# Optimization experiments

Hardware: AMD Instinct MI355X
Metric: run time of the kernel (lower is better)

## Reference

```python
import jax, jax.numpy as jnp
import numpy as np
from jax import lax

DIM = 192
HEADS = 8
WIN = 16
B, H, W = 4, 256, 256


def setup_inputs() -> dict:
    key = jax.random.key(0)
    ks = jax.random.split(key, 8)
    s = 0.02
    return {
        "x": jax.random.normal(ks[0], (B, H, W, DIM), dtype=jnp.float32),
        "ln_g": jnp.ones((DIM,), jnp.float32),
        "ln_b": jnp.zeros((DIM,), jnp.float32),
        "wq1": jax.random.normal(ks[1], (DIM, DIM), jnp.float32) * s,
        "wq2": jax.random.normal(ks[2], (DIM, 1, 3, 3), jnp.float32) * s,
        "wk1": jax.random.normal(ks[3], (DIM, DIM), jnp.float32) * s,
        "wk2": jax.random.normal(ks[4], (DIM, 1, 3, 3), jnp.float32) * s,
        "wv1": jax.random.normal(ks[5], (DIM, DIM), jnp.float32) * s,
        "wv2": jax.random.normal(ks[6], (DIM, 1, 3, 3), jnp.float32) * s,
        "rescale": jnp.ones((HEADS, 1, 1), jnp.float32),
        "w_out": jax.random.normal(ks[7], (DIM, DIM), jnp.float32) * s,
    }


def _layernorm(x, g, b, eps=1e-5):
    mu = jnp.mean(x, axis=-1, keepdims=True)
    var = jnp.var(x, axis=-1, keepdims=True)
    return (x - mu) * lax.rsqrt(var + eps) * g + b


def _qkv(x_nchw, w1, w2):
    # 1x1 pointwise conv (no bias) as GEMM, then 3x3 depthwise conv (groups=dim)
    y = jnp.einsum('oi,bihw->bohw', w1, x_nchw)
    return lax.conv_general_dilated(
        y, w2, window_strides=(1, 1), padding='SAME',
        feature_group_count=DIM,
        dimension_numbers=('NCHW', 'OIHW', 'NCHW'))


def _windows(t):
    # [b,c,H,W] -> [b, nW, heads, d, n]   (nW = num_h*num_w, n = Wh*Ww)
    b = t.shape[0]
    nh, nw = H // WIN, W // WIN
    t = t.reshape(b, DIM, nh, WIN, nw, WIN)
    t = t.transpose(0, 1, 2, 4, 3, 5).reshape(b, DIM, nh * nw, WIN * WIN)
    d = DIM // HEADS
    t = t.reshape(b, HEADS, d, nh * nw, WIN * WIN)
    return t.transpose(0, 3, 1, 2, 4)  # b N h d n


def reference(x, ln_g, ln_b, wq1, wq2, wk1, wk2, wv1, wv2, rescale, w_out):
    b, h, w, c = x.shape
    xn = _layernorm(x, ln_g, ln_b)
    xc = xn.transpose(0, 3, 1, 2)  # NCHW
    q = _windows(_qkv(xc, wq1, wq2))
    k = _windows(_qkv(xc, wk1, wk2))
    v = _windows(_qkv(xc, wv1, wv2))
    # spectral (channel-wise) attention inside each window
    sim = jnp.einsum('bNhin,bNhjn->bNhij', q, k) * rescale
    attn = jax.nn.softmax(sim, axis=-1)
    out = jnp.einsum('bNhij,bNhjn->bNhin', attn, v)  # [b,N,h,d,n]
    # merge heads, un-window
    nh, nw = h // WIN, w // WIN
    out = out.transpose(0, 2, 3, 1, 4).reshape(b, c, nh * nw, WIN * WIN)
    out = out.reshape(b, c, nh, nw, WIN, WIN).transpose(0, 1, 2, 4, 3, 5).reshape(b, c, h, w)
    out = jnp.einsum('oi,bihw->bohw', w_out, out)
    return out.transpose(0, 2, 3, 1)  # [b,h,w,c]
```

## Files before the change

kernel.cpp:

```cpp
#include <hip/hip_runtime.h>
#include <hip/hip_bf16.h>

#define CH    192
#define NB    4
#define NHH   256
#define NWW   256
#define NPOS  (NB*NHH*NWW)
#define HEADS 8
#define DH    24
#define WIN   16
#define PS    ((size_t)NPOS*DH)

typedef unsigned short u16;
typedef __bf16 bf16x8 __attribute__((ext_vector_type(8)));
typedef float  f32x4  __attribute__((ext_vector_type(4)));
typedef u16    u16x8  __attribute__((ext_vector_type(8)));
typedef u16    u16x4  __attribute__((ext_vector_type(4)));

__device__ __forceinline__ float b2f(u16 h) {
    union { unsigned int u; float f; } x; x.u = ((unsigned int)h) << 16; return x.f;
}
__device__ __forceinline__ u16 f2b(float f) {
    union { float f; unsigned int u; } x; x.f = f;
    return (u16)((x.u + 0x7fffu + ((x.u >> 16) & 1u)) >> 16);
}

__global__ __launch_bounds__(256) void prep_weights(
    const float* __restrict__ w0, const float* __restrict__ w1,
    const float* __restrict__ w2, const float* __restrict__ w3,
    u16* __restrict__ pack)
{
    const int t = blockIdx.x * 256 + threadIdx.x;
    const int lane = t & 63, g = t >> 6;
    const int mat = g / 72;
    const float* w = (mat == 0) ? w0 : (mat == 1) ? w1 : (mat == 2) ? w2 : w3;
    const int nt = (g / 6) % 12, ks = g % 6;
    const float* src = w + (nt*16 + (lane & 15)) * CH + ks*32 + (lane >> 4) * 8;
    const float4 a = *(const float4*)(src);
    const float4 b = *(const float4*)(src + 4);
    u16x8 o;
    o[0]=f2b(a.x); o[1]=f2b(a.y); o[2]=f2b(a.z); o[3]=f2b(a.w);
    o[4]=f2b(b.x); o[5]=f2b(b.y); o[6]=f2b(b.z); o[7]=f2b(b.w);
    *(u16x8*)(pack + (size_t)g*512 + lane*8) = o;
}

__global__ __launch_bounds__(256, 6) void ln_qkv_gemm(
    const float* __restrict__ x, const float* __restrict__ lng, const float* __restrict__ lnb,
    const u16* __restrict__ bpack,
    u16* __restrict__ y0, u16* __restrict__ y1, u16* __restrict__ y2)
{
    __shared__ __align__(16) u16 At[32*192];
    __shared__ __align__(16) u16 St32[32*200];
    const int t = threadIdx.x, l = t & 63, w = t >> 6;
    const int lr = l & 15, lg = l >> 4;
    const size_t p0 = (size_t)blockIdx.x * 32;

    {
        const int row = t >> 3, part = t & 7;
        const float* xp = x + (p0 + row) * CH + part * 24;
        float vals[24];
#pragma unroll
        for (int j = 0; j < 6; ++j) {
            float4 v4 = *(const float4*)(xp + j * 4);
            vals[j*4+0]=v4.x; vals[j*4+1]=v4.y; vals[j*4+2]=v4.z; vals[j*4+3]=v4.w;
        }
        float s = 0.f, s2 = 0.f;
#pragma unroll
        for (int j = 0; j < 24; ++j) { s += vals[j]; s2 += vals[j]*vals[j]; }
        s += __shfl_xor(s, 1);  s2 += __shfl_xor(s2, 1);
        s += __shfl_xor(s, 2);  s2 += __shfl_xor(s2, 2);
        s += __shfl_xor(s, 4);  s2 += __shfl_xor(s2, 4);
        const float mu = s * (1.f/192.f);
        const float rs = rsqrtf(s2 * (1.f/192.f) - mu*mu + 1e-5f);
#pragma unroll
        for (int jb = 0; jb < 3; ++jb) {
            u16x8 o;
#pragma unroll
            for (int j = 0; j < 8; ++j) {
                const int c = part*24 + jb*8 + j;
                o[j] = f2b((vals[jb*8+j] - mu) * rs * lng[c] + lnb[c]);
            }
            const int cb = part*3 + jb;
            *(u16x8*)&At[row*192 + (cb ^ (row & 7))*8] = o;
        }
    }
    __syncthreads();

    for (int mat = 0; mat < 3; ++mat) {
        u16* yb = (mat == 0) ? y0 : (mat == 1) ? y1 : y2;
        f32x4 acc[2][3];
#pragma unroll
        for (int mt = 0; mt < 2; ++mt)
#pragma unroll
            for (int nt = 0; nt < 3; ++nt) acc[mt][nt] = (f32x4){0.f,0.f,0.f,0.f};
        const u16* bp = bpack + (size_t)mat*36864 + (size_t)w*3*3072 + l*8;
#pragma unroll
        for (int ks = 0; ks < 6; ++ks) {
            bf16x8 wf[3], xf[2];
#pragma unroll
            for (int nt = 0; nt < 3; ++nt)
                wf[nt] = *(const bf16x8*)(bp + (size_t)nt*3072 + ks*512);
#pragma unroll
            for (int mt = 0; mt < 2; ++mt)
                xf[mt] = *(const bf16x8*)&At[(mt*16 + lr)*192 + ((ks*4 + lg) ^ (lr & 7))*8];
#pragma unroll
            for (int mt = 0; mt < 2; ++mt)
#pragma unroll
                for (int nt = 0; nt < 3; ++nt)
                    acc[mt][nt] = __builtin_amdgcn_mfma_f32_16x16x32_bf16(
                        wf[nt], xf[mt], acc[mt][nt], 0, 0, 0);
        }
        __syncthreads();
#pragma unroll
        for (int mt = 0; mt < 2; ++mt)
#pragma unroll
            for (int nt = 0; nt < 3; ++nt) {
                u16x4 pk;
                pk[0] = f2b(acc[mt][nt][0]); pk[1] = f2b(acc[mt][nt][1]);
                pk[2] = f2b(acc[mt][nt][2]); pk[3] = f2b(acc[mt][nt][3]);
                *(u16x4*)&St32[(mt*16 + lr)*200 + (w*3 + nt)*16 + lg*4] = pk;
            }
        __syncthreads();
        {
            const int hh = t >> 5, r = t & 31;
            u16* dst = yb + (size_t)hh*PS + (p0 + r)*DH;
#pragma unroll
            for (int j8 = 0; j8 < 3; ++j8)
                *(u16x8*)(dst + j8*8) = *(const u16x8*)&St32[r*200 + hh*24 + j8*8];
        }
    }
}

__global__ __launch_bounds__(256) void dwconv_all(
    const u16* __restrict__ in0, const u16* __restrict__ in1, const u16* __restrict__ in2,
    const float* __restrict__ w0, const float* __restrict__ w1, const float* __restrict__ w2,
    u16* __restrict__ out0, u16* __restrict__ out1, u16* __restrict__ out2)
{
    __shared__ float wloc[DH*9];
    const int z = blockIdx.z;
    const u16* in  = (z == 0) ? in0  : (z == 1) ? in1  : in2;
    const float* wdw = (z == 0) ? w0 : (z == 1) ? w1 : w2;
    u16* out       = (z == 0) ? out0 : (z == 1) ? out1 : out2;
    const int t = threadIdx.x;
    const int h = blockIdx.y;
    if (t < DH*9) wloc[t] = wdw[h*DH*9 + t];
    __syncthreads();
    const int NSLICE = NPOS*3/256;
    const int CPX = NSLICE/8;
    const int bx = blockIdx.x;
    const int swz = (bx & 7)*CPX + (bx >> 3);
    const int gid2 = swz * 256 + t;
    const int p  = gid2 / 3, c8 = gid2 - p*3;
    const int x = p & 255, y = (p >> 8) & 255, b = p >> 16;
    const size_t plane = (size_t)h * PS;
    float acc[8] = {0,0,0,0,0,0,0,0};
#pragma unroll
    for (int ky = 0; ky < 3; ++ky) {
        const int yy = y + ky - 1;
        if (yy < 0 || yy >= NHH) continue;
#pragma unroll
        for (int kx = 0; kx < 3; ++kx) {
            const int xx = x + kx - 1;
            if (xx < 0 || xx >= NWW) continue;
            const u16x8 iv = *(const u16x8*)(in + plane + (size_t)((b*NHH + yy)*NWW + xx)*DH + c8*8);
#pragma unroll
            for (int j = 0; j < 8; ++j)
                acc[j] += b2f(iv[j]) * wloc[(c8*8 + j)*9 + ky*3 + kx];
        }
    }
    u16x8 ov;
#pragma unroll
    for (int j = 0; j < 8; ++j) ov[j] = f2b(acc[j]);
    *(u16x8*)(out + plane + (size_t)p*DH + c8*8) = ov;
}

__global__ __launch_bounds__(256) void attn_kernel(
    const u16* __restrict__ q, const u16* __restrict__ k, const u16* __restrict__ v,
    const float* __restrict__ rescale, u16* __restrict__ out)
{
    __shared__ float qt[DH][260];
    __shared__ float kt[DH][260];
    float* pbuf = &kt[0][0];
    const int t    = threadIdx.x;
    const int widx = blockIdx.x;
    const int h    = blockIdx.y;
    const int b  = widx >> 8;
    const int wy = (widx >> 4) & 15, wx = widx & 15;
    const int n  = t;
    const int gy = wy*WIN + (n >> 4), gx = wx*WIN + (n & 15);
    const size_t pbase = (size_t)h*PS + (size_t)((b*NHH + gy)*NWW + gx) * DH;

#pragma unroll
    for (int j8 = 0; j8 < 3; ++j8) {
        const u16x8 qv = *(const u16x8*)(q + pbase + j8*8);
        const u16x8 kv = *(const u16x8*)(k + pbase + j8*8);
#pragma unroll
        for (int j = 0; j < 8; ++j) { qt[j8*8+j][n] = b2f(qv[j]); kt[j8*8+j][n] = b2f(kv[j]); }
    }
    __syncthreads();

    const int wvi  = t >> 6;
    const int lane = t & 63;
    const int i0 = (lane >> 3) * 3, j0 = (lane & 7) * 3;
    float s[3][3];
#pragma unroll
    for (int a2 = 0; a2 < 3; ++a2)
#pragma unroll
        for (int c = 0; c < 3; ++c) s[a2][c] = 0.f;
    for (int nn = wvi*64; nn < wvi*64 + 64; nn += 4) {
        float4 qv[3], kv[3];
#pragma unroll
        for (int a2 = 0; a2 < 3; ++a2) {
            qv[a2] = *(const float4*)&qt[i0+a2][nn];
            kv[a2] = *(const float4*)&kt[j0+a2][nn];
        }
#pragma unroll
        for (int a2 = 0; a2 < 3; ++a2)
#pragma unroll
            for (int c = 0; c < 3; ++c)
                s[a2][c] += qv[a2].x*kv[c].x + qv[a2].y*kv[c].y + qv[a2].z*kv[c].z + qv[a2].w*kv[c].w;
    }
    __syncthreads();

#pragma unroll
    for (int a2 = 0; a2 < 3; ++a2)
#pragma unroll
        for (int c = 0; c < 3; ++c)
            pbuf[wvi*576 + (i0+a2)*24 + (j0+c)] = s[a2][c];
#pragma unroll
    for (int j8 = 0; j8 < 3; ++j8) {
        const u16x8 vv = *(const u16x8*)(v + pbase + j8*8);
#pragma unroll
        for (int j = 0; j < 8; ++j) qt[j8*8+j][n] = b2f(vv[j]);
    }
    __syncthreads();

    const float rsc = rescale[h];
    for (int e = t; e < 576; e += 256) {
        const float sum = pbuf[e] + pbuf[576+e] + pbuf[1152+e] + pbuf[1728+e];
        pbuf[2304 + e] = sum * rsc;
    }
    __syncthreads();

    if (t < 24) {
        float* srow = pbuf + 2304 + t*24;
        float m = srow[0];
#pragma unroll
        for (int j = 1; j < 24; ++j) m = fmaxf(m, srow[j]);
        float ssum = 0.f;
#pragma unroll
        for (int j = 0; j < 24; ++j) { const float e_ = expf(srow[j] - m); srow[j] = e_; ssum += e_; }
        const float inv = 1.f / ssum;
#pragma unroll
        for (int j = 0; j < 24; ++j) srow[j] *= inv;
    }
    __syncthreads();

    const int nc = t & 63;
    const int ib = (t >> 6) * 6;
    float4 acc[6];
#pragma unroll
    for (int ii = 0; ii < 6; ++ii) acc[ii] = make_float4(0.f,0.f,0.f,0.f);
#pragma unroll
    for (int j = 0; j < 24; ++j) {
        const float4 vj = *(const float4*)&qt[j][nc*4];
        const float aw0 = pbuf[2304 + (ib+0)*24 + j];
        const float aw1 = pbuf[2304 + (ib+1)*24 + j];
        const float aw2 = pbuf[2304 + (ib+2)*24 + j];
        const float aw3 = pbuf[2304 + (ib+3)*24 + j];
        const float aw4 = pbuf[2304 + (ib+4)*24 + j];
        const float aw5 = pbuf[2304 + (ib+5)*24 + j];
        acc[0].x += aw0*vj.x; acc[0].y += aw0*vj.y; acc[0].z += aw0*vj.z; acc[0].w += aw0*vj.w;
        acc[1].x += aw1*vj.x; acc[1].y += aw1*vj.y; acc[1].z += aw1*vj.z; acc[1].w += aw1*vj.w;
        acc[2].x += aw2*vj.x; acc[2].y += aw2*vj.y; acc[2].z += aw2*vj.z; acc[2].w += aw2*vj.w;
        acc[3].x += aw3*vj.x; acc[3].y += aw3*vj.y; acc[3].z += aw3*vj.z; acc[3].w += aw3*vj.w;
        acc[4].x += aw4*vj.x; acc[4].y += aw4*vj.y; acc[4].z += aw4*vj.z; acc[4].w += aw4*vj.w;
        acc[5].x += aw5*vj.x; acc[5].y += aw5*vj.y; acc[5].z += aw5*vj.z; acc[5].w += aw5*vj.w;
    }
    __syncthreads();
#pragma unroll
    for (int ii = 0; ii < 6; ++ii)
        *(float4*)&qt[ib+ii][nc*4] = acc[ii];
    __syncthreads();
#pragma unroll
    for (int j8 = 0; j8 < 3; ++j8) {
        u16x8 o;
#pragma unroll
        for (int j = 0; j < 8; ++j) o[j] = f2b(qt[j8*8+j][n]);
        *(u16x8*)(out + pbase + j8*8) = o;
    }
}

__global__ __launch_bounds__(256) void outproj_gemm(
    const u16* __restrict__ a, const u16* __restrict__ bpack, float* __restrict__ yf)
{
    __shared__ __align__(16) u16 At[64*192];
    __shared__ __align__(16) float Sf[32*196];
    const int t = threadIdx.x, l = t & 63, w = t >> 6;
    const int lr = l & 15, lg = l >> 4;
    const size_t p0 = (size_t)blockIdx.x * 64;

#pragma unroll
    for (int i = 0; i < 6; ++i) {
        const int idx = t + i*256;
        const int h = idx / 192;
        const int rem = idx - h*192;
        const int r = rem / 3, c8 = rem - r*3;
        const u16x8 vv = *(const u16x8*)(a + (size_t)h*PS + (p0 + r)*DH + c8*8);
        *(u16x8*)&At[r*192 + (((h*3 + c8) ^ (r & 7))*8)] = vv;
    }
    __syncthreads();

    f32x4 acc[4][3];
#pragma unroll
    for (int mt = 0; mt < 4; ++mt)
#pragma unroll
        for (int nt = 0; nt < 3; ++nt) acc[mt][nt] = (f32x4){0.f,0.f,0.f,0.f};
    const u16* bp = bpack + (size_t)3*36864 + (size_t)w*3*3072 + l*8;
#pragma unroll
    for (int ks = 0; ks < 6; ++ks) {
        bf16x8 af[4], bfr[3];
#pragma unroll
        for (int nt = 0; nt < 3; ++nt)
            bfr[nt] = *(const bf16x8*)(bp + (size_t)nt*3072 + ks*512);
#pragma unroll
        for (int mt = 0; mt < 4; ++mt)
            af[mt] = *(const bf16x8*)&At[(mt*16 + lr)*192 + ((ks*4 + lg) ^ (lr & 7))*8];
#pragma unroll
        for (int mt = 0; mt < 4; ++mt)
#pragma unroll
            for (int nt = 0; nt < 3; ++nt)
                acc[mt][nt] = __builtin_amdgcn_mfma_f32_16x16x32_bf16(
                    af[mt], bfr[nt], acc[mt][nt], 0, 0, 0);
    }
#pragma unroll
    for (int h2 = 0; h2 < 2; ++h2) {
        if (h2) __syncthreads();
#pragma unroll
        for (int mi = 0; mi < 2; ++mi) {
            const int mt = h2*2 + mi;
#pragma unroll
            for (int nt = 0; nt < 3; ++nt)
#pragma unroll
                for (int reg = 0; reg < 4; ++reg)
                    Sf[(mi*16 + lg*4 + reg)*196 + (w*3 + nt)*16 + lr] = acc[mt][nt][reg];
        }
        __syncthreads();
#pragma unroll
        for (int i = 0; i < 6; ++i) {
            const int f = t + i*256;
            const int row = f / 48, c4 = f - row*48;
            *(float4*)(yf + (p0 + h2*32 + row)*CH + c4*4) = *(const float4*)&Sf[row*196 + c4*4];
        }
    }
}

extern "C" void kernel_launch(void* const* d_in, const int* in_sizes, int n_in,
                              void* d_out, int out_size, void* d_ws, size_t ws_size,
                              hipStream_t stream)
{
    (void)in_sizes; (void)n_in; (void)out_size; (void)ws_size;
    const float* x     = (const float*)d_in[0];
    const float* ln_g  = (const float*)d_in[1];
    const float* ln_b  = (const float*)d_in[2];
    const float* wq1   = (const float*)d_in[3];
    const float* wq2   = (const float*)d_in[4];
    const float* wk1   = (const float*)d_in[5];
    const float* wk2   = (const float*)d_in[6];
    const float* wv1   = (const float*)d_in[7];
    const float* wv2   = (const float*)d_in[8];
    const float* rsc   = (const float*)d_in[9];
    const float* w_out = (const float*)d_in[10];
    float* out = (float*)d_out;

    const size_t NT = (size_t)NPOS * CH;
    u16* u1 = (u16*)d_ws;
    u16* u2 = u1 + NT;
    u16* u3 = u2 + NT;
    u16* u4 = u3 + NT;
    u16* u5 = u4 + NT;
    u16* u6 = u5 + NT;
    u16* pack = u6 + NT;

    prep_weights<<<72, 256, 0, stream>>>(wq1, wk1, wv1, w_out, pack);
    ln_qkv_gemm<<<NPOS/32, 256, 0, stream>>>(x, ln_g, ln_b, pack, u1, u2, u3);
    dwconv_all<<<dim3(NPOS*3/256, HEADS, 3), 256, 0, stream>>>(
        u1, u2, u3, wq2, wk2, wv2, u4, u5, u6);
    attn_kernel<<<dim3(NB*256, HEADS), 256, 0, stream>>>(u4, u5, u6, rsc, u1);
    outproj_gemm<<<NPOS/64, 256, 0, stream>>>(u1, pack, out);
}
```

Before: 602.1 us.

## Fuse depthwise 3x3 conv into windowed attention kernel with LDS halo tiles

Merges the separate depthwise-conv kernel into the attention kernel. Each block loads an 18x18 halo tile per tensor into LDS and computes q, k and v convolutions on chip. This removes writing and rereading three full bf16 intermediate tensors and drops one launch. The cost is redundant halo loads, more LDS per block (occupancy is capped via launch bounds), and serialized halo/conv phases. The v halo load is overlapped with the q·k product.

Result: faster. 568.5 us (-5.6%).

```diff
diff --git a/kernel.cpp b/kernel.cpp
--- a/kernel.cpp
+++ b/kernel.cpp
@@ -131,73 +131,80 @@
     }
 }
 
-__global__ __launch_bounds__(256) void dwconv_all(
-    const u16* __restrict__ in0, const u16* __restrict__ in1, const u16* __restrict__ in2,
-    const float* __restrict__ w0, const float* __restrict__ w1, const float* __restrict__ w2,
-    u16* __restrict__ out0, u16* __restrict__ out1, u16* __restrict__ out2)
-{
-    __shared__ float wloc[DH*9];
-    const int z = blockIdx.z;
-    const u16* in  = (z == 0) ? in0  : (z == 1) ? in1  : in2;
-    const float* wdw = (z == 0) ? w0 : (z == 1) ? w1 : w2;
-    u16* out       = (z == 0) ? out0 : (z == 1) ? out1 : out2;
+__global__ __launch_bounds__(256, 2) void dwattn_kernel(
+    const u16* __restrict__ q, const u16* __restrict__ k, const u16* __restrict__ v,
+    const float* __restrict__ wq2, const float* __restrict__ wk2, const float* __restrict__ wv2,
+    const float* __restrict__ rescale, u16* __restrict__ out,
+    const u16* __restrict__ zpage)
+{
+    __shared__ __align__(16) u16 H[7776];
+    __shared__ __align__(16) float qt[24*260];
+    __shared__ __align__(16) float kt[24*260];
+    __shared__ __align__(16) float wloc[3*216];
+    float* pbuf = kt;
+
     const int t = threadIdx.x;
+    const int bx = blockIdx.x;
+    const int widx = (bx & 7)*128 + (bx >> 3);
     const int h = blockIdx.y;
-    if (t < DH*9) wloc[t] = wdw[h*DH*9 + t];
-    __syncthreads();
-    const int NSLICE = NPOS*3/256;
-    const int CPX = NSLICE/8;
-    const int bx = blockIdx.x;
-    const int swz = (bx & 7)*CPX + (bx >> 3);
-    const int gid2 = swz * 256 + t;
-    const int p  = gid2 / 3, c8 = gid2 - p*3;
-    const int x = p & 255, y = (p >> 8) & 255, b = p >> 16;
+    const int b = widx >> 8;
+    const int wy = (widx >> 4) & 15, wx = widx & 15;
     const size_t plane = (size_t)h * PS;
-    float acc[8] = {0,0,0,0,0,0,0,0};
-#pragma unroll
-    for (int ky = 0; ky < 3; ++ky) {
-        const int yy = y + ky - 1;
-        if (yy < 0 || yy >= NHH) continue;
-#pragma unroll
-        for (int kx = 0; kx < 3; ++kx) {
-            const int xx = x + kx - 1;
-            if (xx < 0 || xx >= NWW) continue;
-            const u16x8 iv = *(const u16x8*)(in + plane + (size_t)((b*NHH + yy)*NWW + xx)*DH + c8*8);
-#pragma unroll
-            for (int j = 0; j < 8; ++j)
-                acc[j] += b2f(iv[j]) * wloc[(c8*8 + j)*9 + ky*3 + kx];
-        }
-    }
-    u16x8 ov;
-#pragma unroll
-    for (int j = 0; j < 8; ++j) ov[j] = f2b(acc[j]);
-    *(u16x8*)(out + plane + (size_t)p*DH + c8*8) = ov;
-}
-
-__global__ __launch_bounds__(256) void attn_kernel(
-    const u16* __restrict__ q, const u16* __restrict__ k, const u16* __restrict__ v,
-    const float* __restrict__ rescale, u16* __restrict__ out)
-{
-    __shared__ float qt[DH][260];
-    __shared__ float kt[DH][260];
-    float* pbuf = &kt[0][0];
-    const int t    = threadIdx.x;
-    const int widx = blockIdx.x;
-    const int h    = blockIdx.y;
-    const int b  = widx >> 8;
-    const int wy = (widx >> 4) & 15, wx = widx & 15;
-    const int n  = t;
-    const int gy = wy*WIN + (n >> 4), gx = wx*WIN + (n & 15);
-    const size_t pbase = (size_t)h*PS + (size_t)((b*NHH + gy)*NWW + gx) * DH;
-
-#pragma unroll
-    for (int j8 = 0; j8 < 3; ++j8) {
-        const u16x8 qv = *(const u16x8*)(q + pbase + j8*8);
-        const u16x8 kv = *(const u16x8*)(k + pbase + j8*8);
-#pragma unroll
-        for (int j = 0; j < 8; ++j) { qt[j8*8+j][n] = b2f(qv[j]); kt[j8*8+j][n] = b2f(kv[j]); }
-    }
-    __syncthreads();
+
+    for (int i = t; i < 648; i += 256) {
+        const int tsr = i / 216, r = i - tsr*216;
+        const int c = r / 9, tap = r - c*9;
+        const float* ws = (tsr == 0) ? wq2 : (tsr == 1) ? wk2 : wv2;
+        wloc[tsr*216 + tap*24 + c] = ws[h*216 + c*9 + tap];
+    }
+
+    auto halo = [&](const u16* __restrict__ src) {
+#pragma unroll
+        for (int it = 0; it < 4; ++it) {
+            const int i = t + it*256;
+            if (i < 972) {
+                const int hrow = i / 54, chunk = i - hrow*54;
+                const int px = chunk / 3, c8 = chunk - px*3;
+                const int gy = wy*WIN + hrow - 1, gx = wx*WIN + px - 1;
+                const bool ok = (gy >= 0) && (gy < NHH) && (gx >= 0) && (gx < NWW);
+                const u16* sp = ok ? (src + plane + (size_t)((b*NHH + gy)*NWW + gx)*DH + c8*8)
+                                   : zpage;
+                *(u16x8*)&H[c8*2592 + hrow*144 + px*8] = *(const u16x8*)sp;
+            }
+        }
+    };
+    auto dwc = [&](int tsr, float* __restrict__ dst) {
+        const int py = t >> 4, pxx = t & 15;
+#pragma unroll
+        for (int c8 = 0; c8 < 3; ++c8) {
+            float acc[8] = {0,0,0,0,0,0,0,0};
+#pragma unroll
+            for (int ky = 0; ky < 3; ++ky)
+#pragma unroll
+            for (int kx = 0; kx < 3; ++kx) {
+                const u16x8 hv = *(const u16x8*)&H[c8*2592 + (py+ky)*144 + (pxx+kx)*8];
+                const float* wr = &wloc[tsr*216 + (ky*3 + kx)*24 + c8*8];
+                float w8[8];
+                *(float4*)&w8[0] = *(const float4*)wr;
+                *(float4*)&w8[4] = *(const float4*)(wr + 4);
+#pragma unroll
+                for (int j = 0; j < 8; ++j) acc[j] += b2f(hv[j]) * w8[j];
+            }
+#pragma unroll
+            for (int j = 0; j < 8; ++j) dst[(c8*8 + j)*260 + t] = acc[j];
+        }
+    };
+
+    halo(q);
+    __syncthreads();
+    dwc(0, qt);
+    __syncthreads();
+    halo(k);
+    __syncthreads();
+    dwc(1, kt);
+    __syncthreads();
+
+    halo(v);
 
     const int wvi  = t >> 6;
     const int lane = t & 63;
@@ -211,8 +218,8 @@
         float4 qv[3], kv[3];
 #pragma unroll
         for (int a2 = 0; a2 < 3; ++a2) {
-            qv[a2] = *(const float4*)&qt[i0+a2][nn];
-            kv[a2] = *(const float4*)&kt[j0+a2][nn];
+            qv[a2] = *(const float4*)&qt[(i0+a2)*260 + nn];
+            kv[a2] = *(const float4*)&kt[(j0+a2)*260 + nn];
         }
 #pragma unroll
         for (int a2 = 0; a2 < 3; ++a2)
@@ -227,12 +234,7 @@
 #pragma unroll
         for (int c = 0; c < 3; ++c)
             pbuf[wvi*576 + (i0+a2)*24 + (j0+c)] = s[a2][c];
-#pragma unroll
-    for (int j8 = 0; j8 < 3; ++j8) {
-        const u16x8 vv = *(const u16x8*)(v + pbase + j8*8);
-#pragma unroll
-        for (int j = 0; j < 8; ++j) qt[j8*8+j][n] = b2f(vv[j]);
-    }
+    dwc(2, qt);
     __syncthreads();
 
     const float rsc = rescale[h];
@@ -263,7 +265,7 @@
     for (int ii = 0; ii < 6; ++ii) acc[ii] = make_float4(0.f,0.f,0.f,0.f);
 #pragma unroll
     for (int j = 0; j < 24; ++j) {
-        const float4 vj = *(const float4*)&qt[j][nc*4];
+        const float4 vj = *(const float4*)&qt[j*260 + nc*4];
         const float aw0 = pbuf[2304 + (ib+0)*24 + j];
         const float aw1 = pbuf[2304 + (ib+1)*24 + j];
         const float aw2 = pbuf[2304 + (ib+2)*24 + j];
@@ -280,13 +282,16 @@
     __syncthreads();
 #pragma unroll
     for (int ii = 0; ii < 6; ++ii)
-        *(float4*)&qt[ib+ii][nc*4] = acc[ii];
-    __syncthreads();
+        *(float4*)&qt[(ib+ii)*260 + nc*4] = acc[ii];
+    __syncthreads();
+    const int n = t;
+    const int gy2 = wy*WIN + (n >> 4), gx2 = wx*WIN + (n & 15);
+    const size_t pbase = plane + (size_t)((b*NHH + gy2)*NWW + gx2) * DH;
 #pragma unroll
     for (int j8 = 0; j8 < 3; ++j8) {
         u16x8 o;
 #pragma unroll
-        for (int j = 0; j < 8; ++j) o[j] = f2b(qt[j8*8+j][n]);
+        for (int j = 0; j < 8; ++j) o[j] = f2b(qt[(j8*8+j)*260 + n]);
         *(u16x8*)(out + pbase + j8*8) = o;
     }
 }
@@ -378,14 +383,13 @@
     u16* u2 = u1 + NT;
     u16* u3 = u2 + NT;
     u16* u4 = u3 + NT;
-    u16* u5 = u4 + NT;
-    u16* u6 = u5 + NT;
-    u16* pack = u6 + NT;
-
+    u16* pack = u4 + NT;
+    u16* zpage = pack + 147456;
+
+    hipMemsetAsync(zpage, 0, 512, stream);
     prep_weights<<<72, 256, 0, stream>>>(wq1, wk1, wv1, w_out, pack);
     ln_qkv_gemm<<<NPOS/32, 256, 0, stream>>>(x, ln_g, ln_b, pack, u1, u2, u3);
-    dwconv_all<<<dim3(NPOS*3/256, HEADS, 3), 256, 0, stream>>>(
-        u1, u2, u3, wq2, wk2, wv2, u4, u5, u6);
-    attn_kernel<<<dim3(NB*256, HEADS), 256, 0, stream>>>(u4, u5, u6, rsc, u1);
-    outproj_gemm<<<NPOS/64, 256, 0, stream>>>(u1, pack, out);
-}
+    dwattn_kernel<<<dim3(1024, HEADS), 256, 0, stream>>>(
+        u1, u2, u3, wq2, wk2, wv2, rsc, u4, zpage);
+    outproj_gemm<<<NPOS/64, 256, 0, stream>>>(u4, pack, out);
+}
```
